# Kernel tuning notes

Hardware: AMD Instinct MI355X
Metric: run time of the kernel (lower is better)

The kernel has to match this reference:

```python
import jax, jax.numpy as jnp
import numpy as np

N_HEADS = 16

def setup_inputs() -> dict:
    key = jax.random.key(0)
    k1, k2, k3, k4 = jax.random.split(key, 4)
    B, S, H = 2, 2048, 1024
    x = jax.random.normal(k1, (B, S, H), dtype=jnp.float32)
    pos_table = jax.random.normal(k2, (S, H), dtype=jnp.float32) * 0.02
    W_qkv = jax.random.normal(k3, (H, 3 * H), dtype=jnp.float32) * (1.0 / np.sqrt(H))
    W_out = jax.random.normal(k4, (H, H), dtype=jnp.float32) * (1.0 / np.sqrt(H))
    return {"x": x, "pos_table": pos_table, "W_qkv": W_qkv, "W_out": W_out}


def reference(x, pos_table, W_qkv, W_out):
    B, S, Hd = x.shape
    nh = N_HEADS
    hs = Hd // nh  # head_size
    NEG_INF = jnp.float32(-10000.0)

    pos = pos_table[:S][None, :, :]  # [1, S, H]
    # q, k come from (x + pos_emb); v comes from x alone (duplicate projection)
    qk_proj = (x + pos) @ W_qkv              # [B, S, 3H]
    q = qk_proj[..., :Hd]
    k = qk_proj[..., Hd:2 * Hd]
    v = x @ W_qkv[:, 2 * Hd:]                # [B, S, H]

    def split_heads(t):  # [B, S, H] -> [B, nh, S, hs]
        return t.reshape(B, S, nh, hs).transpose(0, 2, 1, 3)

    q, k, v = split_heads(q), split_heads(k), split_heads(v)

    scores = jnp.einsum('bhqd,bhkd->bhqk', q, k) / jnp.sqrt(jnp.float32(hs))
    q_ind = jnp.arange(S)[:, None]
    k_ind = jnp.arange(S)[None, :]
    mask = q_ind < k_ind  # True where future (masked)
    scores = jnp.where(mask, NEG_INF, scores)

    probs = jax.nn.softmax(scores, axis=-1)
    out = jnp.einsum('bhqk,bhkd->bhqd', probs, v)  # [B, nh, S, hs]
    out = out.transpose(0, 2, 1, 3).reshape(B, S, Hd)
    return out @ W_out
```

## Files before the change

kernel.cpp:

```cpp
#include <hip/hip_runtime.h>

#define SEQ     2048
#define HDIM    1024
#define TOKENS  4096
#define NHEADS  16
#define HS      64
#define LP      72

typedef __bf16 v8bf __attribute__((ext_vector_type(8)));
typedef float  v4f  __attribute__((ext_vector_type(4)));

#define MFMA16(a, b, c) __builtin_amdgcn_mfma_f32_16x16x32_bf16((a), (b), (c), 0, 0, 0)

#define QSCALE (0.125f * 1.44269504088896f)

__device__ __forceinline__ unsigned short f2bf(float f) {
  unsigned int u = __float_as_uint(f);
  u += 0x7FFFu + ((u >> 16) & 1u);
  return (unsigned short)(u >> 16);
}

__device__ __forceinline__ void async16(const void* g, void* l) {
  __builtin_amdgcn_global_load_lds(
      (const __attribute__((address_space(1))) void*)g,
      (__attribute__((address_space(3))) void*)l, 16, 0, 0);
}

__global__ __launch_bounds__(256) void prep_all_kernel(
    const float* __restrict__ x, const float* __restrict__ pos,
    const float* __restrict__ Wqkv, const float* __restrict__ Wout,
    unsigned short* __restrict__ X, unsigned short* __restrict__ XP,
    unsigned short* __restrict__ WQT, unsigned short* __restrict__ WOT) {
  __shared__ float tile[32][33];
  const int id = blockIdx.x;
  if (id < 4096) {
    const int i = (id * 256 + threadIdx.x) * 4;
    float4 xv = *(const float4*)(x + i);
    float4 pv = *(const float4*)(pos + (i & (SEQ * HDIM - 1)));
    ushort4 a, b;
    a.x = f2bf(xv.x); a.y = f2bf(xv.y); a.z = f2bf(xv.z); a.w = f2bf(xv.w);
    b.x = f2bf(xv.x + pv.x); b.y = f2bf(xv.y + pv.y);
    b.z = f2bf(xv.z + pv.z); b.w = f2bf(xv.w + pv.w);
    *(ushort4*)(X + i) = a;
    *(ushort4*)(XP + i) = b;
    return;
  }
  const float* in; unsigned short* out; int R, C, bx, by;
  if (id < 7168) {
    const int t2 = id - 4096;
    in = Wqkv; out = WQT; R = HDIM; C = 3 * HDIM;
    bx = (t2 % 96) * 32; by = (t2 / 96) * 32;
  } else {
    const int t3 = id - 7168;
    in = Wout; out = WOT; R = HDIM; C = HDIM;
    bx = (t3 & 31) * 32; by = (t3 >> 5) * 32;
  }
  const int tx = threadIdx.x & 31, ty = threadIdx.x >> 5;
#pragma unroll
  for (int j = 0; j < 32; j += 8)
    tile[ty + j][tx] = in[(size_t)(by + ty + j) * C + bx + tx];
  __syncthreads();
#pragma unroll
  for (int j = 0; j < 32; j += 8)
    out[(size_t)(bx + ty + j) * R + by + tx] = f2bf(tile[tx][ty + j]);
}

__global__ __launch_bounds__(256) void gemm_qkv_kernel(
    const unsigned short* __restrict__ XP, const unsigned short* __restrict__ X,
    const unsigned short* __restrict__ Wt,
    unsigned short* __restrict__ Qb, unsigned short* __restrict__ Kb,
    unsigned short* __restrict__ VTb) {
  __shared__ unsigned short SM[17408];
  unsigned short* As = SM;
  unsigned short* Bs = SM + 4096;
  const int m0 = blockIdx.x * 128;
  const int n0 = blockIdx.y * 128;
  const unsigned short* A = (n0 < 2 * HDIM) ? XP : X;
  const int t = threadIdx.x;
  const int lane = t & 63, w = t >> 6;
  const int wm = (w >> 1) * 64, wn = (w & 1) * 64;
  const int quad = lane >> 4, l15 = lane & 15;

  v4f acc[4][4] = {};

  const int rowA = t >> 2;
  const int colA = (t & 3) * 8;
  const unsigned short* gA = A + (size_t)(m0 + rowA) * HDIM + colA;
  const unsigned short* gB = Wt + (size_t)(n0 + rowA) * HDIM + colA;
  unsigned short* lA = &As[t * 8];
  unsigned short* lB = &Bs[t * 8];

  for (int k0 = 0; k0 < HDIM; k0 += 32) {
    __syncthreads();
    async16(gA + k0, lA);
    async16(gA + 64 * HDIM + k0, lA + 64 * 32);
    async16(gB + k0, lB);
    async16(gB + 64 * HDIM + k0, lB + 64 * 32);
    __syncthreads();
    v8bf a[4], b[4];
#pragma unroll
    for (int i = 0; i < 4; i++)
      a[i] = *(const v8bf*)&As[(wm + i * 16 + l15) * 32 + quad * 8];
#pragma unroll
    for (int i = 0; i < 4; i++)
      b[i] = *(const v8bf*)&Bs[(wn + i * 16 + l15) * 32 + quad * 8];
#pragma unroll
    for (int i = 0; i < 4; i++)
#pragma unroll
      for (int j = 0; j < 4; j++)
        acc[i][j] = MFMA16(a[i], b[j], acc[i][j]);
  }

  const int b_ = m0 >> 11;
  const int s0 = m0 & (SEQ - 1);

  if (n0 >= 2 * HDIM) {
    unsigned short* St = SM;
    __syncthreads();
#pragma unroll
    for (int i = 0; i < 4; i++)
#pragma unroll
      for (int j = 0; j < 4; j++) {
        ushort4 u;
        u.x = f2bf(acc[i][j][0]); u.y = f2bf(acc[i][j][1]);
        u.z = f2bf(acc[i][j][2]); u.w = f2bf(acc[i][j][3]);
        *(ushort4*)&St[(wn + j * 16 + l15) * 136 + wm + i * 16 + quad * 4] = u;
      }
    __syncthreads();
#pragma unroll
    for (int it = 0; it < 8; it++) {
      const int lin = it * 256 + t;
      const int n = lin >> 4, s8 = (lin & 15) * 8;
      const int c2 = (n0 - 2 * HDIM) + n;
      const int h = c2 >> 6, d = c2 & 63;
      *(uint4*)(VTb + ((size_t)(((b_ << 4) | h) * HS + d)) * SEQ + s0 + s8) =
          *(const uint4*)&St[n * 136 + s8];
    }
  } else {
    const float scale = (n0 < HDIM) ? QSCALE : 1.0f;
    unsigned short* dst = (n0 < HDIM) ? Qb : Kb;
#pragma unroll
    for (int i = 0; i < 4; i++) {
#pragma unroll
      for (int j = 0; j < 4; j++) {
#pragma unroll
        for (int r = 0; r < 4; r++) {
          const int s_ = s0 + wm + i * 16 + quad * 4 + r;
          const int c2 = (n0 & (HDIM - 1)) + wn + j * 16 + l15;
          const int h = c2 >> 6, d = c2 & 63;
          dst[((size_t)(((b_ << 4) | h) * SEQ + s_)) * HS + d] =
              f2bf(acc[i][j][r] * scale);
        }
      }
    }
  }
}

__global__ __launch_bounds__(256, 2) void attn_pair_kernel(
    const unsigned short* __restrict__ Qp, const unsigned short* __restrict__ Kp,
    const unsigned short* __restrict__ Vp, unsigned short* __restrict__ ATTN) {
  __shared__ unsigned short Qs[128 * LP];
  __shared__ unsigned short Ks[64 * LP];
  __shared__ unsigned short Vs[64 * LP];
  __shared__ unsigned short Ps[4][32 * LP];

  const int p  = blockIdx.x;
  const int bh = blockIdx.y;
  const int b_ = bh >> 4, h = bh & 15;
  const int qlo = p, qhi = 31 - p;
  const int q0lo = qlo * 64, q0hi = qhi * 64;
  const int t = threadIdx.x;
  const int lane = t & 63, w = t >> 6;
  const int quad = lane >> 4, l15 = lane & 15;

  const unsigned short* Qg = Qp + (size_t)bh * SEQ * HS;
  const unsigned short* Kg = Kp + (size_t)bh * SEQ * HS;
  const unsigned short* Vg = Vp + (size_t)bh * HS * SEQ;

  const int sr = t >> 3, scol = (t & 7) * 8;
  *(uint4*)&Qs[sr * LP + scol] = *(const uint4*)(Qg + (size_t)(q0lo + sr) * HS + scol);
  *(uint4*)&Qs[(sr + 32) * LP + scol] =
      *(const uint4*)(Qg + (size_t)(q0lo + sr + 32) * HS + scol);
  *(uint4*)&Qs[(sr + 64) * LP + scol] =
      *(const uint4*)(Qg + (size_t)(q0hi + sr) * HS + scol);
  *(uint4*)&Qs[(sr + 96) * LP + scol] =
      *(const uint4*)(Qg + (size_t)(q0hi + sr + 32) * HS + scol);
  __syncthreads();

  v8bf bq[2][2];
#pragma unroll
  for (int tl = 0; tl < 2; tl++)
#pragma unroll
    for (int kh = 0; kh < 2; kh++)
      bq[tl][kh] = *(const v8bf*)&Qs[(tl * 64 + w * 16 + l15) * LP + kh * 32 + quad * 8];

  v8bf ones;
#pragma unroll
  for (int j = 0; j < 8; j++) ones[j] = (__bf16)1.0f;

  v4f o[2][4] = {};
  v4f lacc[2] = {};

  uint4 kr0, kr1, vr0, vr1;
  kr0 = *(const uint4*)(Kg + (size_t)sr * HS + scol);
  kr1 = *(const uint4*)(Kg + (size_t)(sr + 32) * HS + scol);
  vr0 = *(const uint4*)(Vg + (size_t)sr * SEQ + scol);
  vr1 = *(const uint4*)(Vg + (size_t)(sr + 32) * SEQ + scol);

  const int qrow_hi = q0hi + w * 16 + l15;
  const int qrow_lo = q0lo + w * 16 + l15;

  for (int cI = 0; cI <= qhi; cI++) {
    const int kc = cI * 64;
    __syncthreads();
    *(uint4*)&Ks[sr * LP + scol] = kr0;
    *(uint4*)&Ks[(sr + 32) * LP + scol] = kr1;
    *(uint4*)&Vs[sr * LP + scol] = vr0;
    *(uint4*)&Vs[(sr + 32) * LP + scol] = vr1;
    if (cI < qhi) {
      const int kn = kc + 64;
      kr0 = *(const uint4*)(Kg + (size_t)(kn + sr) * HS + scol);
      kr1 = *(const uint4*)(Kg + (size_t)(kn + sr + 32) * HS + scol);
      vr0 = *(const uint4*)(Vg + (size_t)sr * SEQ + kn + scol);
      vr1 = *(const uint4*)(Vg + (size_t)(sr + 32) * SEQ + kn + scol);
    }
    __syncthreads();

    v8bf kf0[4], kf1[4];
#pragma unroll
    for (int ni = 0; ni < 4; ni++) {
      kf0[ni] = *(const v8bf*)&Ks[(ni * 16 + l15) * LP + quad * 8];
      kf1[ni] = *(const v8bf*)&Ks[(ni * 16 + l15) * LP + 32 + quad * 8];
    }

    const bool doLo = (cI <= qlo);

    {
      v4f sc[4] = {};
#pragma unroll
      for (int ni = 0; ni < 4; ni++) {
        sc[ni] = MFMA16(kf0[ni], bq[1][0], sc[ni]);
        sc[ni] = MFMA16(kf1[ni], bq[1][1], sc[ni]);
      }
      if (cI == qhi) {
#pragma unroll
        for (int ni = 0; ni < 4; ni++) {
          const int key = kc + ni * 16 + quad * 4;
#pragma unroll
          for (int r = 0; r < 4; r++)
            if (key + r > qrow_hi) sc[ni][r] = -1e30f;
        }
      }
#pragma unroll
      for (int ni = 0; ni < 4; ni++) {
        const float p0 = exp2f(sc[ni][0]), p1 = exp2f(sc[ni][1]);
        const float p2 = exp2f(sc[ni][2]), p3 = exp2f(sc[ni][3]);
        uint2 pk;
        pk.x = __builtin_amdgcn_perm(__float_as_uint(p1), __float_as_uint(p0), 0x07060302u);
        pk.y = __builtin_amdgcn_perm(__float_as_uint(p3), __float_as_uint(p2), 0x07060302u);
        *(uint2*)&Ps[w][(16 + l15) * LP + ni * 16 + quad * 4] = pk;
      }
    }
    if (doLo) {
      v4f sc[4] = {};
#pragma unroll
      for (int ni = 0; ni < 4; ni++) {
        sc[ni] = MFMA16(kf0[ni], bq[0][0], sc[ni]);
        sc[ni] = MFMA16(kf1[ni], bq[0][1], sc[ni]);
      }
      if (cI == qlo) {
#pragma unroll
        for (int ni = 0; ni < 4; ni++) {
          const int key = kc + ni * 16 + quad * 4;
#pragma unroll
          for (int r = 0; r < 4; r++)
            if (key + r > qrow_lo) sc[ni][r] = -1e30f;
        }
      }
#pragma unroll
      for (int ni = 0; ni < 4; ni++) {
        const float p0 = exp2f(sc[ni][0]), p1 = exp2f(sc[ni][1]);
        const float p2 = exp2f(sc[ni][2]), p3 = exp2f(sc[ni][3]);
        uint2 pk;
        pk.x = __builtin_amdgcn_perm(__float_as_uint(p1), __float_as_uint(p0), 0x07060302u);
        pk.y = __builtin_amdgcn_perm(__float_as_uint(p3), __float_as_uint(p2), 0x07060302u);
        *(uint2*)&Ps[w][l15 * LP + ni * 16 + quad * 4] = pk;
      }
    }

#pragma unroll
    for (int ki = 0; ki < 2; ki++) {
      v8bf pahi = *(const v8bf*)&Ps[w][(16 + l15) * LP + ki * 32 + quad * 8];
      lacc[1] = MFMA16(pahi, ones, lacc[1]);
      v8bf palo;
      if (doLo) {
        palo = *(const v8bf*)&Ps[w][l15 * LP + ki * 32 + quad * 8];
        lacc[0] = MFMA16(palo, ones, lacc[0]);
      }
#pragma unroll
      for (int ni = 0; ni < 4; ni++) {
        v8bf vb = *(const v8bf*)&Vs[(ni * 16 + l15) * LP + ki * 32 + quad * 8];
        o[1][ni] = MFMA16(pahi, vb, o[1][ni]);
        if (doLo) o[0][ni] = MFMA16(palo, vb, o[0][ni]);
      }
    }
  }

#pragma unroll
  for (int tl = 0; tl < 2; tl++) {
    const int q0 = tl ? q0hi : q0lo;
    const int row_base = q0 + w * 16 + quad * 4;
    float invl[4];
#pragma unroll
    for (int r = 0; r < 4; r++) invl[r] = 1.0f / lacc[tl][r];
#pragma unroll
    for (int ni = 0; ni < 4; ni++)
#pragma unroll
      for (int r = 0; r < 4; r++) {
        const int tr = b_ * SEQ + row_base + r;
        ATTN[(size_t)tr * HDIM + h * HS + ni * 16 + l15] = f2bf(o[tl][ni][r] * invl[r]);
      }
  }
}

__global__ __launch_bounds__(256) void gemm_out_kernel(
    const unsigned short* __restrict__ Ab, const unsigned short* __restrict__ Wt,
    float* __restrict__ out) {
  __shared__ unsigned short As[128 * 32];
  __shared__ unsigned short Bs[128 * 32];
  const int m0 = blockIdx.x * 128;
  const int n0 = blockIdx.y * 128;
  const int t = threadIdx.x;
  const int lane = t & 63, w = t >> 6;
  const int wm = (w >> 1) * 64, wn = (w & 1) * 64;
  const int quad = lane >> 4, l15 = lane & 15;

  v4f acc[4][4] = {};

  const int rowA = t >> 2;
  const int colA = (t & 3) * 8;
  const unsigned short* gA = Ab + (size_t)(m0 + rowA) * HDIM + colA;
  const unsigned short* gB = Wt + (size_t)(n0 + rowA) * HDIM + colA;
  unsigned short* lA = &As[t * 8];
  unsigned short* lB = &Bs[t * 8];

  for (int k0 = 0; k0 < HDIM; k0 += 32) {
    __syncthreads();
    async16(gA + k0, lA);
    async16(gA + 64 * HDIM + k0, lA + 64 * 32);
    async16(gB + k0, lB);
    async16(gB + 64 * HDIM + k0, lB + 64 * 32);
    __syncthreads();
    v8bf a[4], b[4];
#pragma unroll
    for (int i = 0; i < 4; i++)
      a[i] = *(const v8bf*)&As[(wm + i * 16 + l15) * 32 + quad * 8];
#pragma unroll
    for (int i = 0; i < 4; i++)
      b[i] = *(const v8bf*)&Bs[(wn + i * 16 + l15) * 32 + quad * 8];
#pragma unroll
    for (int i = 0; i < 4; i++)
#pragma unroll
      for (int j = 0; j < 4; j++)
        acc[i][j] = MFMA16(a[i], b[j], acc[i][j]);
  }

#pragma unroll
  for (int i = 0; i < 4; i++) {
#pragma unroll
    for (int j = 0; j < 4; j++) {
#pragma unroll
      for (int r = 0; r < 4; r++) {
        const int tr = m0 + wm + i * 16 + quad * 4 + r;
        const int c = n0 + wn + j * 16 + l15;
        out[(size_t)tr * HDIM + c] = acc[i][j][r];
      }
    }
  }
}

extern "C" void kernel_launch(void* const* d_in, const int* in_sizes, int n_in,
                              void* d_out, int out_size, void* d_ws, size_t ws_size,
                              hipStream_t stream) {
  (void)in_sizes; (void)n_in; (void)out_size; (void)ws_size;
  const float* x    = (const float*)d_in[0];
  const float* pos  = (const float*)d_in[1];
  const float* Wqkv = (const float*)d_in[2];
  const float* Wout = (const float*)d_in[3];
  float* out = (float*)d_out;

  char* ws = (char*)d_ws;
  unsigned short* XP   = (unsigned short*)(ws);
  unsigned short* X    = (unsigned short*)(ws + ((size_t)8  << 20));
  unsigned short* WQT  = (unsigned short*)(ws + ((size_t)16 << 20));
  unsigned short* WOT  = (unsigned short*)(ws + ((size_t)22 << 20));
  unsigned short* Qb   = (unsigned short*)(ws + ((size_t)24 << 20));
  unsigned short* Kb   = (unsigned short*)(ws + ((size_t)32 << 20));
  unsigned short* VTb  = (unsigned short*)(ws + ((size_t)40 << 20));
  unsigned short* ATTN = (unsigned short*)(ws + ((size_t)48 << 20));

  prep_all_kernel<<<8192, 256, 0, stream>>>(x, pos, Wqkv, Wout, X, XP, WQT, WOT);

  dim3 g1(TOKENS / 128, 3 * HDIM / 128);
  gemm_qkv_kernel<<<g1, 256, 0, stream>>>(XP, X, WQT, Qb, Kb, VTb);

  dim3 g2(16, 2 * NHEADS);
  attn_pair_kernel<<<g2, 256, 0, stream>>>(Qb, Kb, VTb, ATTN);

  dim3 g3(TOKENS / 128, HDIM / 128);
  gemm_out_kernel<<<g3, 256, 0, stream>>>(ATTN, WOT, out);
}
```

Baseline: 198.7 us.

## Swap MFMA operands for V transpose, reorder attention grid, shrink out-GEMM tile

For the V projection, the QKV GEMM swaps the MFMA operands so the accumulator comes out already transposed. VT is then stored straight from registers, which drops the LDS staging pass and its two barriers, but the global stores become scattered 2-byte writes. The attention grid is reordered so adjacent blocks cover different heads for the same query pair, which changes scheduling and cache locality. The output GEMM uses 128x64 tiles instead of 128x128, doubling the block count to 512 for better CU occupancy at the cost of less B-tile reuse per block.

```diff
diff --git a/kernel.cpp b/kernel.cpp
--- a/kernel.cpp
+++ b/kernel.cpp
@@ -70,12 +70,12 @@
     const unsigned short* __restrict__ Wt,
     unsigned short* __restrict__ Qb, unsigned short* __restrict__ Kb,
     unsigned short* __restrict__ VTb) {
-  __shared__ unsigned short SM[17408];
-  unsigned short* As = SM;
-  unsigned short* Bs = SM + 4096;
+  __shared__ unsigned short As[128 * 32];
+  __shared__ unsigned short Bs[128 * 32];
   const int m0 = blockIdx.x * 128;
   const int n0 = blockIdx.y * 128;
-  const unsigned short* A = (n0 < 2 * HDIM) ? XP : X;
+  const bool isV = (n0 >= 2 * HDIM);
+  const unsigned short* A = isV ? X : XP;
   const int t = threadIdx.x;
   const int lane = t & 63, w = t >> 6;
   const int wm = (w >> 1) * 64, wn = (w & 1) * 64;
@@ -104,37 +104,37 @@
 #pragma unroll
     for (int i = 0; i < 4; i++)
       b[i] = *(const v8bf*)&Bs[(wn + i * 16 + l15) * 32 + quad * 8];
-#pragma unroll
-    for (int i = 0; i < 4; i++)
-#pragma unroll
-      for (int j = 0; j < 4; j++)
-        acc[i][j] = MFMA16(a[i], b[j], acc[i][j]);
+    if (isV) {
+#pragma unroll
+      for (int i = 0; i < 4; i++)
+#pragma unroll
+        for (int j = 0; j < 4; j++)
+          acc[i][j] = MFMA16(b[j], a[i], acc[i][j]);
+    } else {
+#pragma unroll
+      for (int i = 0; i < 4; i++)
+#pragma unroll
+        for (int j = 0; j < 4; j++)
+          acc[i][j] = MFMA16(a[i], b[j], acc[i][j]);
+    }
   }
 
   const int b_ = m0 >> 11;
   const int s0 = m0 & (SEQ - 1);
 
-  if (n0 >= 2 * HDIM) {
-    unsigned short* St = SM;
-    __syncthreads();
-#pragma unroll
-    for (int i = 0; i < 4; i++)
+  if (isV) {
+#pragma unroll
+    for (int i = 0; i < 4; i++) {
 #pragma unroll
       for (int j = 0; j < 4; j++) {
-        ushort4 u;
-        u.x = f2bf(acc[i][j][0]); u.y = f2bf(acc[i][j][1]);
-        u.z = f2bf(acc[i][j][2]); u.w = f2bf(acc[i][j][3]);
-        *(ushort4*)&St[(wn + j * 16 + l15) * 136 + wm + i * 16 + quad * 4] = u;
-      }
-    __syncthreads();
-#pragma unroll
-    for (int it = 0; it < 8; it++) {
-      const int lin = it * 256 + t;
-      const int n = lin >> 4, s8 = (lin & 15) * 8;
-      const int c2 = (n0 - 2 * HDIM) + n;
-      const int h = c2 >> 6, d = c2 & 63;
-      *(uint4*)(VTb + ((size_t)(((b_ << 4) | h) * HS + d)) * SEQ + s0 + s8) =
-          *(const uint4*)&St[n * 136 + s8];
+        const int s_ = s0 + wm + i * 16 + l15;
+#pragma unroll
+        for (int r = 0; r < 4; r++) {
+          const int c2 = (n0 - 2 * HDIM) + wn + j * 16 + quad * 4 + r;
+          const int h = c2 >> 6, d = c2 & 63;
+          VTb[((size_t)(((b_ << 4) | h) * HS + d)) * SEQ + s_] = f2bf(acc[i][j][r]);
+        }
+      }
     }
   } else {
     const float scale = (n0 < HDIM) ? QSCALE : 1.0f;
@@ -164,8 +164,8 @@
   __shared__ unsigned short Vs[64 * LP];
   __shared__ unsigned short Ps[4][32 * LP];
 
-  const int p  = blockIdx.x;
-  const int bh = blockIdx.y;
+  const int bh = blockIdx.x;
+  const int p  = blockIdx.y;
   const int b_ = bh >> 4, h = bh & 15;
   const int qlo = p, qhi = 31 - p;
   const int q0lo = qlo * 64, q0hi = qhi * 64;
@@ -327,15 +327,15 @@
     const unsigned short* __restrict__ Ab, const unsigned short* __restrict__ Wt,
     float* __restrict__ out) {
   __shared__ unsigned short As[128 * 32];
-  __shared__ unsigned short Bs[128 * 32];
+  __shared__ unsigned short Bs[64 * 32];
   const int m0 = blockIdx.x * 128;
-  const int n0 = blockIdx.y * 128;
+  const int n0 = blockIdx.y * 64;
   const int t = threadIdx.x;
   const int lane = t & 63, w = t >> 6;
-  const int wm = (w >> 1) * 64, wn = (w & 1) * 64;
+  const int wm = w * 32;
   const int quad = lane >> 4, l15 = lane & 15;
 
-  v4f acc[4][4] = {};
+  v4f acc[2][4] = {};
 
   const int rowA = t >> 2;
   const int colA = (t & 3) * 8;
@@ -348,31 +348,30 @@
     __syncthreads();
     async16(gA + k0, lA);
     async16(gA + 64 * HDIM + k0, lA + 64 * 32);
-    async16(gB + k0, lB);
-    async16(gB + 64 * HDIM + k0, lB + 64 * 32);
-    __syncthreads();
-    v8bf a[4], b[4];
-#pragma unroll
-    for (int i = 0; i < 4; i++)
+    if (rowA < 64) async16(gB + k0, lB);
+    __syncthreads();
+    v8bf a[2], b[4];
+#pragma unroll
+    for (int i = 0; i < 2; i++)
       a[i] = *(const v8bf*)&As[(wm + i * 16 + l15) * 32 + quad * 8];
 #pragma unroll
-    for (int i = 0; i < 4; i++)
-      b[i] = *(const v8bf*)&Bs[(wn + i * 16 + l15) * 32 + quad * 8];
-#pragma unroll
-    for (int i = 0; i < 4; i++)
+    for (int j = 0; j < 4; j++)
+      b[j] = *(const v8bf*)&Bs[(j * 16 + l15) * 32 + quad * 8];
+#pragma unroll
+    for (int i = 0; i < 2; i++)
 #pragma unroll
       for (int j = 0; j < 4; j++)
         acc[i][j] = MFMA16(a[i], b[j], acc[i][j]);
   }
 
 #pragma unroll
-  for (int i = 0; i < 4; i++) {
+  for (int i = 0; i < 2; i++) {
 #pragma unroll
     for (int j = 0; j < 4; j++) {
 #pragma unroll
       for (int r = 0; r < 4; r++) {
         const int tr = m0 + wm + i * 16 + quad * 4 + r;
-        const int c = n0 + wn + j * 16 + l15;
+        const int c = n0 + j * 16 + l15;
         out[(size_t)tr * HDIM + c] = acc[i][j][r];
       }
     }
@@ -404,9 +403,9 @@
   dim3 g1(TOKENS / 128, 3 * HDIM / 128);
   gemm_qkv_kernel<<<g1, 256, 0, stream>>>(XP, X, WQT, Qb, Kb, VTb);
 
-  dim3 g2(16, 2 * NHEADS);
+  dim3 g2(2 * NHEADS, 16);
   attn_pair_kernel<<<g2, 256, 0, stream>>>(Qb, Kb, VTb, ATTN);
 
-  dim3 g3(TOKENS / 128, HDIM / 128);
+  dim3 g3(TOKENS / 128, HDIM / 64);
   gemm_out_kernel<<<g3, 256, 0, stream>>>(ATTN, WOT, out);
 }
```

New measurement: 191.4 us. 1.04x faster.
